# Optimization experiments

Measured on AMD Instinct MI355X. Metric: run time of the kernel, lower is better.

Reference implementation:

```python
import math
import jax, jax.numpy as jnp
import numpy as np

B, T, D, K, H, L = 16384, 64, 32, 32, 32, 16
EPS = 1e-5

def _dct_basis(num_basis, horizon):
    # Type-II DCT rows, L2-normalized (matches build_dct_basis)
    n = np.arange(horizon, dtype=np.float32)
    rows = []
    for k in range(num_basis):
        if k == 0:
            rows.append(np.ones(horizon, dtype=np.float32) / math.sqrt(horizon))
        else:
            rows.append(np.sqrt(2.0 / horizon) * np.cos(math.pi * k * (2 * n + 1) / (2 * horizon)).astype(np.float32))
    return np.stack(rows, axis=0)

def setup_inputs() -> dict:
    key = jax.random.key(0)
    ks = jax.random.split(key, 6)
    sample = jax.random.normal(ks[0], (B, T, D), dtype=jnp.float32)
    basis = jnp.asarray(_dct_basis(K, T))                      # [K, T] learnable param, DCT init
    # Stacked per-basis MLP weights (K independent Linear(D,H)->GELU->Linear(H,L))
    W1 = jax.random.uniform(ks[1], (K, D, H), jnp.float32, -1.0, 1.0) / math.sqrt(D)
    b1 = jax.random.uniform(ks[2], (K, H), jnp.float32, -1.0, 1.0) / math.sqrt(D)
    W2 = jax.random.uniform(ks[3], (K, H, L), jnp.float32, -1.0, 1.0) / math.sqrt(H)
    b2 = jax.random.uniform(ks[4], (K, L), jnp.float32, -1.0, 1.0) / math.sqrt(H)
    gamma = jnp.ones((L,), jnp.float32)
    beta = jnp.zeros((L,), jnp.float32)
    return {"sample": sample, "basis": basis, "W1": W1, "b1": b1,
            "W2": W2, "b2": b2, "gamma": gamma, "beta": beta}

def reference(sample, basis, W1, b1, W2, b2, gamma, beta):
    # spectral projection: [B,K,D]
    coeffs = jnp.einsum('kt,btd->bkd', basis, sample)
    # K independent MLPs as one grouped GEMM (block-diagonal view of the ModuleList loop)
    h = jax.nn.gelu(jnp.einsum('bkd,kdh->bkh', coeffs, W1) + b1[None], approximate=False)
    z = jnp.einsum('bkh,khl->bkl', h, W2) + b2[None]           # [B,K,L]
    # LayerNorm over last dim
    mu = jnp.mean(z, axis=-1, keepdims=True)
    var = jnp.mean(jnp.square(z - mu), axis=-1, keepdims=True)
    return gamma * (z - mu) / jnp.sqrt(var + EPS) + beta
```

## Files before the change

kernel.cpp:

```cpp
#include <hip/hip_runtime.h>
#include <hip/hip_bf16.h>
#include <math.h>

#define B_TOT 16384
#define T_DIM 64
#define D_DIM 32
#define K_DIM 32
#define H_DIM 32
#define L_DIM 16

__global__ void prep_transpose(const float* __restrict__ basis, float* __restrict__ basisT) {
    int i = blockIdx.x * blockDim.x + threadIdx.x;
    if (i < K_DIM * T_DIM) {
        int k = i / T_DIM, t = i % T_DIM;
        basisT[t * K_DIM + k] = basis[i];
    }
}

__global__ __launch_bounds__(256) void proj_kernel(const float* __restrict__ sample,
                                                   const float* __restrict__ basisT,
                                                   __hip_bfloat16* __restrict__ coeffs) {
    __shared__ float smp[8 * T_DIM * D_DIM];
    const int tid = threadIdx.x;
    const long b0 = (long)blockIdx.x * 8;

    const float4* src = reinterpret_cast<const float4*>(sample + b0 * (T_DIM * D_DIM));
    float4* dst = reinterpret_cast<float4*>(smp);
#pragma unroll
    for (int i = 0; i < 16; ++i) dst[tid + i * 256] = src[tid + i * 256];
    __syncthreads();

    const int bi = tid >> 5, d = tid & 31;
    float acc[K_DIM];
#pragma unroll
    for (int k = 0; k < K_DIM; ++k) acc[k] = 0.f;

    const float* sp = smp + bi * (T_DIM * D_DIM) + d;
#pragma unroll 4
    for (int t = 0; t < T_DIM; ++t) {
        float sv = sp[t * D_DIM];
        const float* bt = basisT + t * K_DIM;
#pragma unroll
        for (int k = 0; k < K_DIM; ++k) acc[k] = fmaf(bt[k], sv, acc[k]);
    }

    __hip_bfloat16* cp = coeffs + (b0 + bi) * (K_DIM * D_DIM) + d;
#pragma unroll
    for (int k = 0; k < K_DIM; ++k) cp[k * D_DIM] = __float2bfloat16(acc[k]);
}

__global__ __launch_bounds__(256) void mlp_kernel(const __hip_bfloat16* __restrict__ coeffs,
                                                  const float* __restrict__ W1,
                                                  const float* __restrict__ b1,
                                                  const float* __restrict__ W2,
                                                  const float* __restrict__ b2,
                                                  const float* __restrict__ gamma,
                                                  const float* __restrict__ beta,
                                                  float* __restrict__ out) {
    const int tid = threadIdx.x;
    const int lane = tid & 63;
    const int wv = tid >> 6;
    const int bchunk = blockIdx.x >> 3;
    const int kgrp = blockIdx.x & 7;
    int k = kgrp * 4 + wv;
    k = __builtin_amdgcn_readfirstlane(k);
    const long b = (long)bchunk * 64 + lane;

    const uint4* cp4 = reinterpret_cast<const uint4*>(coeffs + (b * K_DIM + k) * D_DIM);
    float cv[D_DIM];
#pragma unroll
    for (int q = 0; q < 4; ++q) {
        uint4 u = cp4[q];
        unsigned int uu[4] = {u.x, u.y, u.z, u.w};
#pragma unroll
        for (int j = 0; j < 4; ++j) {
            cv[q * 8 + j * 2 + 0] = __uint_as_float(uu[j] << 16);
            cv[q * 8 + j * 2 + 1] = __uint_as_float(uu[j] & 0xffff0000u);
        }
    }

    const float* w1p = W1 + k * (D_DIM * H_DIM);
    const float* b1p = b1 + k * H_DIM;
    float h[H_DIM];
#pragma unroll
    for (int j = 0; j < H_DIM; ++j) h[j] = b1p[j];
#pragma unroll 4
    for (int d = 0; d < D_DIM; ++d) {
        const float* wr = w1p + d * H_DIM;
        float c = cv[d];
#pragma unroll
        for (int j = 0; j < H_DIM; ++j) h[j] = fmaf(c, wr[j], h[j]);
    }

#pragma unroll
    for (int j = 0; j < H_DIM; ++j) {
        float u = h[j];
        h[j] = 0.5f * u * (1.0f + erff(u * 0.70710678118654752f));
    }

    const float* w2p = W2 + k * (H_DIM * L_DIM);
    const float* b2p = b2 + k * L_DIM;
    float z[L_DIM];
#pragma unroll
    for (int l = 0; l < L_DIM; ++l) z[l] = b2p[l];
#pragma unroll 4
    for (int hh = 0; hh < H_DIM; ++hh) {
        const float* wr = w2p + hh * L_DIM;
        float hv = h[hh];
#pragma unroll
        for (int l = 0; l < L_DIM; ++l) z[l] = fmaf(hv, wr[l], z[l]);
    }

    float mu = 0.f;
#pragma unroll
    for (int l = 0; l < L_DIM; ++l) mu += z[l];
    mu *= (1.0f / L_DIM);
    float var = 0.f;
#pragma unroll
    for (int l = 0; l < L_DIM; ++l) { float dz = z[l] - mu; var = fmaf(dz, dz, var); }
    var *= (1.0f / L_DIM);
    float rstd = rsqrtf(var + 1e-5f);

    float4 o[4];
    float* of = reinterpret_cast<float*>(o);
#pragma unroll
    for (int l = 0; l < L_DIM; ++l) of[l] = fmaf(gamma[l] * rstd, z[l] - mu, beta[l]);

    float4* op = reinterpret_cast<float4*>(out + (b * K_DIM + k) * L_DIM);
#pragma unroll
    for (int q = 0; q < 4; ++q) op[q] = o[q];
}

extern "C" void kernel_launch(void* const* d_in, const int* in_sizes, int n_in,
                              void* d_out, int out_size, void* d_ws, size_t ws_size,
                              hipStream_t stream) {
    const float* sample = (const float*)d_in[0];
    const float* basis  = (const float*)d_in[1];
    const float* W1     = (const float*)d_in[2];
    const float* b1     = (const float*)d_in[3];
    const float* W2     = (const float*)d_in[4];
    const float* b2     = (const float*)d_in[5];
    const float* gamma  = (const float*)d_in[6];
    const float* beta   = (const float*)d_in[7];
    float* out = (float*)d_out;

    float* basisT = (float*)d_ws;
    __hip_bfloat16* coeffs = (__hip_bfloat16*)((char*)d_ws + 32768);

    prep_transpose<<<8, 256, 0, stream>>>(basis, basisT);
    proj_kernel<<<B_TOT / 8, 256, 0, stream>>>(sample, basisT, coeffs);
    mlp_kernel<<<(B_TOT / 64) * 8, 256, 0, stream>>>(coeffs, W1, b1, W2, b2, gamma, beta, out);
}
```

Before: 269.9 us.

## Use K-major coeffs layout, read sample directly, and add fast erf GELU

The intermediate coeffs move from [B,K,D] to [K,B,D] layout, so the projection kernel writes contiguous rows per k and each MLP block works on a single k across 256 batch items. The projection kernel drops its shared-memory staging and barrier and reads sample straight from global memory, which improves occupancy at the cost of less coalesced, strided loads. GELU's erff is replaced with the Abramowitz-Stegun polynomial, built on a hardware reciprocal and __expf. That approximation has error around 1e-7, which lowers accuracy slightly.

```diff
diff --git a/kernel.cpp b/kernel.cpp
--- a/kernel.cpp
+++ b/kernel.cpp
@@ -8,6 +8,7 @@
 #define K_DIM 32
 #define H_DIM 32
 #define L_DIM 16
+#define KBD (B_TOT * D_DIM)
 
 __global__ void prep_transpose(const float* __restrict__ basis, float* __restrict__ basisT) {
     int i = blockIdx.x * blockDim.x + threadIdx.x;
@@ -20,23 +21,16 @@
 __global__ __launch_bounds__(256) void proj_kernel(const float* __restrict__ sample,
                                                    const float* __restrict__ basisT,
                                                    __hip_bfloat16* __restrict__ coeffs) {
-    __shared__ float smp[8 * T_DIM * D_DIM];
     const int tid = threadIdx.x;
-    const long b0 = (long)blockIdx.x * 8;
+    const int bi = tid >> 5, d = tid & 31;
+    const long b = (long)blockIdx.x * 8 + bi;
 
-    const float4* src = reinterpret_cast<const float4*>(sample + b0 * (T_DIM * D_DIM));
-    float4* dst = reinterpret_cast<float4*>(smp);
-#pragma unroll
-    for (int i = 0; i < 16; ++i) dst[tid + i * 256] = src[tid + i * 256];
-    __syncthreads();
-
-    const int bi = tid >> 5, d = tid & 31;
     float acc[K_DIM];
 #pragma unroll
     for (int k = 0; k < K_DIM; ++k) acc[k] = 0.f;
 
-    const float* sp = smp + bi * (T_DIM * D_DIM) + d;
-#pragma unroll 4
+    const float* sp = sample + b * (T_DIM * D_DIM) + d;
+#pragma unroll 2
     for (int t = 0; t < T_DIM; ++t) {
         float sv = sp[t * D_DIM];
         const float* bt = basisT + t * K_DIM;
@@ -44,9 +38,23 @@
         for (int k = 0; k < K_DIM; ++k) acc[k] = fmaf(bt[k], sv, acc[k]);
     }
 
-    __hip_bfloat16* cp = coeffs + (b0 + bi) * (K_DIM * D_DIM) + d;
+    __hip_bfloat16* cp = coeffs + b * D_DIM + d;
 #pragma unroll
-    for (int k = 0; k < K_DIM; ++k) cp[k * D_DIM] = __float2bfloat16(acc[k]);
+    for (int k = 0; k < K_DIM; ++k) cp[(long)k * KBD] = __float2bfloat16(acc[k]);
+}
+
+__device__ __forceinline__ float gelu_exact(float x) {
+    const float iSqrt2 = 0.70710678118654752f;
+    float y = x * iSqrt2;
+    float ay = fabsf(y);
+    float t = __builtin_amdgcn_rcpf(fmaf(0.3275911f, ay, 1.0f));
+    float p = fmaf(fmaf(fmaf(fmaf(1.061405429f, t, -1.453152027f),
+                             t, 1.421413741f),
+                        t, -0.284496736f),
+                   t, 0.254829592f) * t;
+    float e = 1.0f - p * __expf(-ay * ay);
+    e = copysignf(e, y);
+    return 0.5f * x * (1.0f + e);
 }
 
 __global__ __launch_bounds__(256) void mlp_kernel(const __hip_bfloat16* __restrict__ coeffs,
@@ -58,15 +66,10 @@
                                                   const float* __restrict__ beta,
                                                   float* __restrict__ out) {
     const int tid = threadIdx.x;
-    const int lane = tid & 63;
-    const int wv = tid >> 6;
-    const int bchunk = blockIdx.x >> 3;
-    const int kgrp = blockIdx.x & 7;
-    int k = kgrp * 4 + wv;
-    k = __builtin_amdgcn_readfirstlane(k);
-    const long b = (long)bchunk * 64 + lane;
+    const int k = blockIdx.x >> 6;
+    const long b = (long)(blockIdx.x & 63) * 256 + tid;
 
-    const uint4* cp4 = reinterpret_cast<const uint4*>(coeffs + (b * K_DIM + k) * D_DIM);
+    const uint4* cp4 = reinterpret_cast<const uint4*>(coeffs + (long)k * KBD + b * D_DIM);
     float cv[D_DIM];
 #pragma unroll
     for (int q = 0; q < 4; ++q) {
@@ -93,10 +96,7 @@
     }
 
 #pragma unroll
-    for (int j = 0; j < H_DIM; ++j) {
-        float u = h[j];
-        h[j] = 0.5f * u * (1.0f + erff(u * 0.70710678118654752f));
-    }
+    for (int j = 0; j < H_DIM; ++j) h[j] = gelu_exact(h[j]);
 
     const float* w2p = W2 + k * (H_DIM * L_DIM);
     const float* b2p = b2 + k * L_DIM;
@@ -149,5 +149,5 @@
 
     prep_transpose<<<8, 256, 0, stream>>>(basis, basisT);
     proj_kernel<<<B_TOT / 8, 256, 0, stream>>>(sample, basisT, coeffs);
-    mlp_kernel<<<(B_TOT / 64) * 8, 256, 0, stream>>>(coeffs, W1, b1, W2, b2, gamma, beta, out);
+    mlp_kernel<<<(B_TOT / 256) * K_DIM, 256, 0, stream>>>(coeffs, W1, b1, W2, b2, gamma, beta, out);
 }
```

After: 266.7 us. No clear change (-1.2%).
